# Kernel tuning notes

Hardware: AMD Instinct MI355X
Metric: run time of the kernel (lower is better)

## Reference

```python
import jax, jax.numpy as jnp
import numpy as np

B, S, H = 2, 2048, 1024
NH = 16
HD = H // NH  # 64


def _linear_params(key, fan_in, fan_out):
    k1, k2 = jax.random.split(key)
    bound = 1.0 / np.sqrt(fan_in)
    W = jax.random.uniform(k1, (fan_in, fan_out), jnp.float32, -bound, bound)
    b = jax.random.uniform(k2, (fan_out,), jnp.float32, -bound, bound)
    return W, b


def setup_inputs() -> dict:
    key = jax.random.key(0)
    ks = jax.random.split(key, 7)
    hidden_states = jax.random.normal(ks[0], (B, S, H), jnp.float32)
    governance_embeddings = jax.random.normal(ks[1], (B, H), jnp.float32)
    Wq, bq = _linear_params(ks[2], H, H)
    Wk, bk = _linear_params(ks[3], H, H)
    Wv, bv = _linear_params(ks[4], H, H)
    Wgq, bgq = _linear_params(ks[5], H, H)
    Wgk, bgk = _linear_params(ks[6], H, H)
    return {
        'hidden_states': hidden_states,
        'governance_embeddings': governance_embeddings,
        'Wq': Wq, 'bq': bq, 'Wk': Wk, 'bk': bk, 'Wv': Wv, 'bv': bv,
        'Wgq': Wgq, 'bgq': bgq, 'Wgk': Wgk, 'bgk': bgk,
    }


def reference(hidden_states, governance_embeddings, Wq, bq, Wk, bk, Wv, bv, Wgq, bgq, Wgk, bgk):
    b, s, h = hidden_states.shape
    # QKV projections -> [b, nh, s, hd]
    def heads(x):
        return x.reshape(b, s, NH, HD).transpose(0, 2, 1, 3)
    q = heads(hidden_states @ Wq + bq)
    k = heads(hidden_states @ Wk + bk)
    v = heads(hidden_states @ Wv + bv)

    scale = jnp.float32(1.0 / np.sqrt(HD))
    scores = jnp.einsum('bhid,bhjd->bhij', q, k) * scale  # [b,nh,s,s]

    # governance bias: one query per example vs per-token keys (unscaled)
    gq = (governance_embeddings @ Wgq + bgq).reshape(b, NH, HD)      # [b,nh,hd]
    gk = (hidden_states @ Wgk + bgk).reshape(b, s, NH, HD)           # [b,s,nh,hd]
    gov_scores = jnp.einsum('bhd,bshd->bhs', gq, gk)                 # [b,nh,s]

    # bias is constant along key dim (torch expand on last axis)
    combined = scores + 0.1 * gov_scores[..., :, None]

    probs = jax.nn.softmax(combined, axis=-1)  # dropout = identity (eval)
    context = jnp.einsum('bhij,bhjd->bhid', probs, v)
    context = context.transpose(0, 2, 1, 3).reshape(b, s, h)

    entropy = -jnp.sum(probs * jnp.log(probs + 1e-8), axis=-1).mean()
    influence = jnp.abs(gov_scores).mean()  # mean over expanded tensor == mean over [b,nh,s]
    concentration = probs.max(axis=-1).mean()
    return context, entropy, influence, concentration
```

## Files before the change

kernel.cpp:

```cpp
#include <hip/hip_runtime.h>


typedef unsigned short u16;
typedef __attribute__((ext_vector_type(8))) short bf16x8;
typedef __attribute__((ext_vector_type(4))) float f32x4;
typedef __attribute__((ext_vector_type(16))) float f32x16;
typedef __attribute__((ext_vector_type(2))) float f32x2;
typedef __attribute__((ext_vector_type(4))) u16 u16x4;
typedef __attribute__((ext_vector_type(4))) float float4v;
typedef __attribute__((ext_vector_type(2))) unsigned uint2v;

typedef const __attribute__((address_space(1))) void gvoid_t;
typedef __attribute__((address_space(3))) void lvoid_t;

__device__ __forceinline__ void gl_lds16(const void* g, void* l) {
  __builtin_amdgcn_global_load_lds((gvoid_t*)g, (lvoid_t*)l, 16, 0, 0);
}

__device__ __forceinline__ u16 f2bf(float x) {
  union { float f; unsigned u; } v; v.f = x;
  unsigned r = v.u + 0x7fffu + ((v.u >> 16) & 1u);
  return (u16)(r >> 16);
}
__device__ __forceinline__ float bf2f(u16 h) {
  union { unsigned u; float f; } v; v.u = ((unsigned)h) << 16; return v.f;
}
__device__ __forceinline__ unsigned pk2(float hi, float lo) {
  union { float f; unsigned u; } a, b; a.f = hi; b.f = lo;
  return __builtin_amdgcn_perm(a.u, b.u, 0x07060302u);
}
__device__ __forceinline__ bf16x8 mk8(unsigned a, unsigned b, unsigned c, unsigned d) {
  union { unsigned u[4]; bf16x8 v; } x;
  x.u[0] = a; x.u[1] = b; x.u[2] = c; x.u[3] = d; return x.v;
}

#if defined(__has_builtin)
#if __has_builtin(__builtin_amdgcn_permlane32_swap)
#define HAVE_PLSWAP 1
#endif
#if __has_builtin(__builtin_amdgcn_exp2f)
#define EXP2(x) __builtin_amdgcn_exp2f(x)
#endif
#endif
#ifndef EXP2
#define EXP2(x) exp2f(x)
#endif

__device__ __forceinline__ void plswap(unsigned& a, unsigned& b, int lane) {
#ifdef HAVE_PLSWAP
  uint2v r = __builtin_amdgcn_permlane32_swap(a, b, false, false);
  a = r.x; b = r.y;
#else
  unsigned ca = __builtin_amdgcn_ds_bpermute((lane ^ 32) << 2, a);
  unsigned cb = __builtin_amdgcn_ds_bpermute((lane ^ 32) << 2, b);
  unsigned na = (lane < 32) ? a : cb;
  unsigned nb = (lane < 32) ? ca : b;
  a = na; b = nb;
#endif
}

__global__ void prep(const float* __restrict__ hs,
                     const float* __restrict__ W0, const float* __restrict__ W1,
                     const float* __restrict__ W2, const float* __restrict__ W3,
                     const float* __restrict__ ge, const float* __restrict__ Wgq,
                     u16* __restrict__ hsB, u16* __restrict__ WB,
                     float* __restrict__ gq_part) {
  __shared__ __align__(16) u16 T[64][72];
  int bx = blockIdx.x, tid = threadIdx.x;
  if (bx < 2048) {
    int i = bx * 256 + tid;
    const float4v* in4 = (const float4v*)hs;
    float4v a = in4[i * 2], b = in4[i * 2 + 1];
    bf16x8 v;
    v[0] = (short)f2bf(a.x); v[1] = (short)f2bf(a.y);
    v[2] = (short)f2bf(a.z); v[3] = (short)f2bf(a.w);
    v[4] = (short)f2bf(b.x); v[5] = (short)f2bf(b.y);
    v[6] = (short)f2bf(b.z); v[7] = (short)f2bf(b.w);
    *(bf16x8*)&hsB[(size_t)i * 8] = v;
    return;
  }
  if (bx < 3072) {
    int idx = bx - 2048;
    int mat = idx >> 8, sub = idx & 255;
    const float* W = (mat == 0) ? W0 : (mat == 1) ? W1 : (mat == 2) ? W2 : W3;
    int k0 = (sub >> 4) * 64, n0 = (sub & 15) * 64;
#pragma unroll
    for (int p = 0; p < 4; ++p) {
      int chunk = p * 256 + tid;
      int row = chunk >> 4, cp = chunk & 15;
      float4v v = *(const float4v*)&W[(size_t)(k0 + row) * 1024 + n0 + cp * 4];
      u16x4 o; o.x = f2bf(v.x); o.y = f2bf(v.y); o.z = f2bf(v.z); o.w = f2bf(v.w);
      *(u16x4*)&T[row][cp * 4] = o;
    }
    __syncthreads();
#pragma unroll
    for (int p = 0; p < 2; ++p) {
      int chunk = p * 256 + tid;
      int nrow = chunk >> 3, cp = chunk & 7;
      bf16x8 v;
#pragma unroll
      for (int e = 0; e < 8; ++e) v[e] = (short)T[cp * 8 + e][nrow];
      *(bf16x8*)&WB[(size_t)(mat * 1024 + n0 + nrow) * 1024 + k0 + cp * 8] = v;
    }
    return;
  }
  {
    int idx = bx - 3072;
    int kb = idx >> 1, b = idx & 1;
    int col0 = tid * 4;
    float4v s = {0.f, 0.f, 0.f, 0.f};
    for (int k = kb * 32; k < kb * 32 + 32; ++k) {
      float g = ge[b * 1024 + k];
      float4v w = *(const float4v*)&Wgq[(size_t)k * 1024 + col0];
      s.x += g * w.x; s.y += g * w.y; s.z += g * w.z; s.w += g * w.w;
    }
    *(float4v*)&gq_part[(size_t)idx * 1024 + col0] = s;
  }
}

__global__ __launch_bounds__(256, 3) void gemm_qkvg(
    const u16* __restrict__ A, const u16* __restrict__ Bw,
    const float* __restrict__ bq, const float* __restrict__ bk,
    const float* __restrict__ bv, const float* __restrict__ bgk,
    const float* __restrict__ bgq, const float* __restrict__ gq_part,
    u16* __restrict__ Qb, u16* __restrict__ Kb,
    u16* __restrict__ GKb, u16* __restrict__ Vt,
    float* __restrict__ gq_final, float* __restrict__ acc3) {
  if (blockIdx.x == 1024) {
    int tid = threadIdx.x;
    if (tid < 3) acc3[tid] = 0.f;
#pragma unroll
    for (int i = 0; i < 8; ++i) {
      int t = tid + i * 256;
      float s = bgq[t & 1023];
      for (int kb = 0; kb < 32; ++kb)
        s += gq_part[(size_t)(kb * 2 + (t >> 10)) * 1024 + (t & 1023)];
      gq_final[t] = s;
    }
    return;
  }
  __shared__ __align__(16) u16 As[2][128 * 32];
  __shared__ __align__(16) u16 Bs[2][128 * 32];
  const int tid = threadIdx.x, lane = tid & 63, wv = tid >> 6;
  const int li = lane & 15, quad = lane >> 4;
  const int bid = blockIdx.x;
  const int nb = bid & 31, mb = bid >> 5;
  const u16* Ap = A + (size_t)(mb * 128) * 1024;
  const u16* Bp = Bw + (size_t)(nb * 128) * 1024;
  const int wm0 = (wv >> 1) * 64, wn0 = (wv & 1) * 64;

  f32x4 acc[4][4];
#pragma unroll
  for (int t = 0; t < 4; ++t)
#pragma unroll
    for (int u = 0; u < 4; ++u) acc[t][u] = (f32x4){0.f, 0.f, 0.f, 0.f};

#pragma unroll
  for (int jj = 0; jj < 2; ++jj) {
    int j = wv * 2 + jj;
    int row = j * 16 + (lane >> 2);
    int co = lane & 3;
    gl_lds16(Ap + (size_t)row * 1024 + co * 8, &As[0][j * 512]);
    gl_lds16(Bp + (size_t)row * 1024 + co * 8, &Bs[0][j * 512]);
  }

  for (int kt = 0; kt < 32; ++kt) {
    const int cur = kt & 1;
    __syncthreads();
    if (kt < 31) {
#pragma unroll
      for (int jj = 0; jj < 2; ++jj) {
        int j = wv * 2 + jj;
        int row = j * 16 + (lane >> 2);
        int co = lane & 3;
        gl_lds16(Ap + (size_t)row * 1024 + (kt + 1) * 32 + co * 8, &As[cur ^ 1][j * 512]);
        gl_lds16(Bp + (size_t)row * 1024 + (kt + 1) * 32 + co * 8, &Bs[cur ^ 1][j * 512]);
      }
    }
    bf16x8 af[4], bf[4];
#pragma unroll
    for (int t = 0; t < 4; ++t)
      af[t] = *(const bf16x8*)&As[cur][(wm0 + t * 16 + li) * 32 + quad * 8];
#pragma unroll
    for (int u = 0; u < 4; ++u)
      bf[u] = *(const bf16x8*)&Bs[cur][(wn0 + u * 16 + li) * 32 + quad * 8];
#pragma unroll
    for (int t = 0; t < 4; ++t)
#pragma unroll
      for (int u = 0; u < 4; ++u)
        acc[t][u] = __builtin_amdgcn_mfma_f32_16x16x32_bf16(af[t], bf[u], acc[t][u], 0, 0, 0);
  }

  const int nbase = nb * 128;
  const int mat = nbase >> 10;
  if (mat == 2) {
#pragma unroll
    for (int t = 0; t < 4; ++t)
#pragma unroll
      for (int u = 0; u < 4; ++u) {
        int col = (nbase & 1023) + wn0 + u * 16 + li;
        float bb = bv[col];
        int row = mb * 128 + wm0 + t * 16 + quad * 4;
        int b = row >> 11, s = row & 2047;
        uint2 w;
        w.x = pk2(acc[t][u][1] + bb, acc[t][u][0] + bb);
        w.y = pk2(acc[t][u][3] + bb, acc[t][u][2] + bb);
        *(uint2*)&Vt[(size_t)b * (1024 * 2048) + (size_t)col * 2048 + s] = w;
      }
  } else {
    const float* bias = (mat == 0) ? bq : (mat == 1) ? bk : bgk;
    u16* outp = (mat == 0) ? Qb : (mat == 1) ? Kb : GKb;
    const float qscale = (mat == 0) ? 0.18033688f : 1.0f;
#pragma unroll
    for (int t = 0; t < 4; ++t)
#pragma unroll
      for (int u = 0; u < 4; ++u) {
        int col = (nbase & 1023) + wn0 + u * 16 + li;
        float bb = bias[col];
#pragma unroll
        for (int r = 0; r < 4; ++r) {
          int row = mb * 128 + wm0 + t * 16 + quad * 4 + r;
          outp[(size_t)row * 1024 + col] = f2bf((acc[t][u][r] + bb) * qscale);
        }
      }
  }
}

__global__ __launch_bounds__(256, 2) void attn_kernel(
    const u16* __restrict__ Qb, const u16* __restrict__ Kb,
    const u16* __restrict__ Vt, float* __restrict__ out,
    float* __restrict__ acc3 ) {
  __shared__ __align__(16) u16 Ks[2][128 * 64];
  __shared__ __align__(16) u16 Vs[2][64 * 128];
  __shared__ float red[8];

  const int tid = threadIdx.x, lane = tid & 63, wv = tid >> 6;
  const int q_l = lane & 31, half = lane >> 5;
  const int bx = blockIdx.x;
  const int bh = bx & 31, qb = bx >> 5;
  const int b = bh >> 4, h = bh & 15;

  const u16* Qp = Qb + (size_t)(b * 2048 + qb * 128 + wv * 32 + q_l) * 1024 + h * 64;
  const u16* Kp = Kb + (size_t)(b * 2048) * 1024 + h * 64;
  const u16* Vp = Vt + (size_t)b * (1024 * 2048) + (size_t)(h * 64) * 2048;

  bf16x8 qf[4];
#pragma unroll
  for (int s = 0; s < 4; ++s)
    qf[s] = *(const bf16x8*)&Qp[s * 16 + half * 8];

  f32x2 mx2 = {-3.0e38f, -3.0e38f}, ps2 = {0.f, 0.f}, es2 = {0.f, 0.f};
  f32x16 accO[2];
#pragma unroll
  for (int dt = 0; dt < 2; ++dt)
#pragma unroll
    for (int r = 0; r < 16; ++r) accO[dt][r] = 0.f;

#pragma unroll
  for (int jj = 0; jj < 4; ++jj) {
    int j = wv * 4 + jj;
    int row = j * 8 + (lane >> 3);
    int c16 = (lane & 7) ^ (row & 7);
    gl_lds16(Kp + (size_t)row * 1024 + c16 * 8, &Ks[0][j * 512]);
  }
#pragma unroll
  for (int jj = 0; jj < 4; ++jj) {
    int j = wv * 4 + jj;
    int row = j * 4 + (lane >> 4);
    int c16 = (lane & 15) ^ (row & 7);
    gl_lds16(Vp + (size_t)row * 2048 + c16 * 8, &Vs[0][j * 512]);
  }

  for (int kt = 0; kt < 16; ++kt) {
    const int cur = kt & 1;
    __syncthreads();
    if (kt < 15) {
      const u16* Kpt = Kp + (size_t)((kt + 1) * 128) * 1024;
#pragma unroll
      for (int jj = 0; jj < 4; ++jj) {
        int j = wv * 4 + jj;
        int row = j * 8 + (lane >> 3);
        int c16 = (lane & 7) ^ (row & 7);
        gl_lds16(Kpt + (size_t)row * 1024 + c16 * 8, &Ks[cur ^ 1][j * 512]);
      }
#pragma unroll
      for (int jj = 0; jj < 4; ++jj) {
        int j = wv * 4 + jj;
        int row = j * 4 + (lane >> 4);
        int c16 = (lane & 15) ^ (row & 7);
        gl_lds16(Vp + (size_t)row * 2048 + (kt + 1) * 128 + c16 * 8, &Vs[cur ^ 1][j * 512]);
      }
    }
    const u16* KsC = &Ks[cur][0];
    const u16* VsC = &Vs[cur][0];

#pragma unroll
    for (int u = 0; u < 4; ++u) {
      f32x16 c;
#pragma unroll
      for (int r = 0; r < 16; ++r) c[r] = 0.f;
#pragma unroll
      for (int s = 0; s < 4; ++s) {
        int p = (2 * s + half) ^ (q_l & 7);
        bf16x8 a = *(const bf16x8*)&KsC[(u * 32 + q_l) * 64 + p * 8];
        c = __builtin_amdgcn_mfma_f32_32x32x16_bf16(a, qf[s], c, 0, 0, 0);
      }
#pragma unroll
      for (int r = 0; r < 8; ++r) {
        f32x2 sv = {c[2 * r], c[2 * r + 1]};
        mx2 = __builtin_elementwise_max(mx2, sv);
        f32x2 pe = {EXP2(sv.x), EXP2(sv.y)};
        ps2 += pe;
        es2 += pe * sv;
        c[2 * r] = pe.x; c[2 * r + 1] = pe.y;
      }
      unsigned p0 = pk2(c[1], c[0]),   p1 = pk2(c[3], c[2]);
      unsigned p2 = pk2(c[5], c[4]),   p3 = pk2(c[7], c[6]);
      unsigned p4 = pk2(c[9], c[8]),   p5 = pk2(c[11], c[10]);
      unsigned p6 = pk2(c[13], c[12]), p7 = pk2(c[15], c[14]);
      plswap(p0, p2, lane); plswap(p1, p3, lane);
      plswap(p4, p6, lane); plswap(p5, p7, lane);
      bf16x8 bf0 = mk8(p0, p1, p2, p3);
      bf16x8 bf1 = mk8(p4, p5, p6, p7);
#pragma unroll
      for (int dt = 0; dt < 2; ++dt) {
        int d = dt * 32 + q_l;
        int pa = (u * 4 + half) ^ (d & 7);
        int pb = (u * 4 + 2 + half) ^ (d & 7);
        bf16x8 av0 = *(const bf16x8*)&VsC[d * 128 + pa * 8];
        accO[dt] = __builtin_amdgcn_mfma_f32_32x32x16_bf16(av0, bf0, accO[dt], 0, 0, 0);
        bf16x8 av1 = *(const bf16x8*)&VsC[d * 128 + pb * 8];
        accO[dt] = __builtin_amdgcn_mfma_f32_32x32x16_bf16(av1, bf1, accO[dt], 0, 0, 0);
      }
    }
  }

  float l_st = ps2.x + ps2.y, e_st = es2.x + es2.y, m_st = fmaxf(mx2.x, mx2.y);
  float lsum = l_st + __shfl_xor(l_st, 32, 64);
  float esum = e_st + __shfl_xor(e_st, 32, 64);
  float mm = fmaxf(m_st, __shfl_xor(m_st, 32, 64));
  float inv = 1.0f / lsum;
  float entw = __logf(lsum) - 0.69314718f * esum * inv;
  float concw = EXP2(mm) * inv;

  float* outp = out + (size_t)(b * 2048 + qb * 128 + wv * 32 + q_l) * 1024 + h * 64;
#pragma unroll
  for (int dt = 0; dt < 2; ++dt)
#pragma unroll
    for (int g = 0; g < 4; ++g) {
      float4v o;
      o.x = accO[dt][4 * g + 0] * inv; o.y = accO[dt][4 * g + 1] * inv;
      o.z = accO[dt][4 * g + 2] * inv; o.w = accO[dt][4 * g + 3] * inv;
      *(float4v*)&outp[dt * 32 + 8 * g + 4 * half] = o;
    }

#pragma unroll
  for (int off = 1; off < 64; off <<= 1) {
    entw += __shfl_xor(entw, off, 64);
    concw += __shfl_xor(concw, off, 64);
  }
  if (lane == 0) { red[wv] = entw * 0.5f; red[4 + wv] = concw * 0.5f; }
  __syncthreads();
  if (tid == 0) {
    atomicAdd(&acc3[0], red[0] + red[1] + red[2] + red[3]);
    atomicAdd(&acc3[1], red[4] + red[5] + red[6] + red[7]);
  }
}

__global__ void gov_kernel(const u16* __restrict__ GKb, const float* __restrict__ gq,
                           float* __restrict__ acc_inf) {
  __shared__ float redI[4];
  int lane = threadIdx.x & 63, wv = threadIdx.x >> 6;
  int wid = blockIdx.x * 4 + wv;
  int b = wid >> 11, s = wid & 2047;
  const u16* gk = GKb + (size_t)(b * 2048 + s) * 1024 + lane * 16;
  const float* gqp = gq + b * 1024 + lane * 16;
  bf16x8 g0 = *(const bf16x8*)gk, g1 = *(const bf16x8*)(gk + 8);
  float4v q0 = *(const float4v*)&gqp[0], q1 = *(const float4v*)&gqp[4];
  float4v q2 = *(const float4v*)&gqp[8], q3 = *(const float4v*)&gqp[12];
  float sum = 0.f;
  sum += bf2f((u16)g0[0]) * q0.x + bf2f((u16)g0[1]) * q0.y +
         bf2f((u16)g0[2]) * q0.z + bf2f((u16)g0[3]) * q0.w;
  sum += bf2f((u16)g0[4]) * q1.x + bf2f((u16)g0[5]) * q1.y +
         bf2f((u16)g0[6]) * q1.z + bf2f((u16)g0[7]) * q1.w;
  sum += bf2f((u16)g1[0]) * q2.x + bf2f((u16)g1[1]) * q2.y +
         bf2f((u16)g1[2]) * q2.z + bf2f((u16)g1[3]) * q2.w;
  sum += bf2f((u16)g1[4]) * q3.x + bf2f((u16)g1[5]) * q3.y +
         bf2f((u16)g1[6]) * q3.z + bf2f((u16)g1[7]) * q3.w;
  sum += __shfl_xor(sum, 1, 64);
  sum += __shfl_xor(sum, 2, 64);
  float v = ((lane & 3) == 0) ? fabsf(sum) : 0.f;
  v += __shfl_xor(v, 4, 64);  v += __shfl_xor(v, 8, 64);
  v += __shfl_xor(v, 16, 64); v += __shfl_xor(v, 32, 64);
  if (lane == 0) redI[wv] = v;
  __syncthreads();
  if (threadIdx.x == 0)
    atomicAdd(acc_inf, redI[0] + redI[1] + redI[2] + redI[3]);
}

__global__ void finalize(const float* __restrict__ acc3, float* __restrict__ out) {
  if (threadIdx.x == 0) {
    out[0] = acc3[0] * (1.f / 65536.f);
    out[1] = acc3[2] * (1.f / 65536.f);
    out[2] = acc3[1] * (1.f / 65536.f);
  }
}

extern "C" void kernel_launch(void* const* d_in, const int* in_sizes, int n_in,
                              void* d_out, int out_size, void* d_ws, size_t ws_size,
                              hipStream_t stream) {
  (void)in_sizes; (void)n_in; (void)out_size; (void)ws_size;
  const float* hs  = (const float*)d_in[0];
  const float* ge  = (const float*)d_in[1];
  const float* Wq  = (const float*)d_in[2];
  const float* bq  = (const float*)d_in[3];
  const float* Wk  = (const float*)d_in[4];
  const float* bk  = (const float*)d_in[5];
  const float* Wv  = (const float*)d_in[6];
  const float* bv  = (const float*)d_in[7];
  const float* Wgq = (const float*)d_in[8];
  const float* bgq = (const float*)d_in[9];
  const float* Wgk = (const float*)d_in[10];
  const float* bgk = (const float*)d_in[11];

  char* ws = (char*)d_ws;
  u16* hsB = (u16*)(ws);
  u16* WB  = (u16*)(ws + (size_t)(8 << 20));
  u16* Qb  = (u16*)(ws + (size_t)(16 << 20));
  u16* Kb  = (u16*)(ws + (size_t)(24 << 20));
  u16* Vt  = (u16*)(ws + (size_t)(32 << 20));
  u16* GKb = (u16*)(ws + (size_t)(40 << 20));
  float* gq_part  = (float*)(ws + (size_t)(48 << 20));
  float* gq_final = (float*)(ws + (size_t)(48 << 20) + 262144);
  float* acc3     = (float*)(ws + (size_t)(48 << 20) + 524288);
  float* out = (float*)d_out;

  prep<<<3136, 256, 0, stream>>>(hs, Wq, Wk, Wv, Wgk, ge, Wgq, hsB, WB, gq_part);
  gemm_qkvg<<<1025, 256, 0, stream>>>(hsB, WB, bq, bk, bv, bgk, bgq, gq_part,
                                      Qb, Kb, GKb, Vt, gq_final, acc3);
  attn_kernel<<<512, 256, 0, stream>>>(Qb, Kb, Vt, out, acc3);
  gov_kernel<<<1024, 256, 0, stream>>>(GKb, gq_final, acc3 + 2);
  finalize<<<1, 64, 0, stream>>>(acc3, out + 4194304);
}
```

Measured before the change: 222.5 us.

## Fuse governance influence reduction into GEMM epilogue and drop permlane swaps in attention

The governance-key projection is no longer written to memory. Its dot product with the governance query and the absolute-value reduction now run in the GEMM epilogue, which removes the separate gov_kernel launch and the GK round trip through global memory. The gq reduction is recomputed per block in the epilogue, and the acc3 zeroing moves into prep. Separately, the attention P·V step drops the permlane32 swaps and instead gathers V fragments as 8-byte LDS reads in the matching order, trading cross-lane swaps for more, smaller LDS loads.

After: 209.5 us. 5.8% less time.

```diff
diff --git a/kernel.cpp b/kernel.cpp
--- a/kernel.cpp
+++ b/kernel.cpp
@@ -8,7 +8,6 @@
 typedef __attribute__((ext_vector_type(2))) float f32x2;
 typedef __attribute__((ext_vector_type(4))) u16 u16x4;
 typedef __attribute__((ext_vector_type(4))) float float4v;
-typedef __attribute__((ext_vector_type(2))) unsigned uint2v;
 
 typedef const __attribute__((address_space(1))) void gvoid_t;
 typedef __attribute__((address_space(3))) void lvoid_t;
@@ -35,9 +34,6 @@
 }
 
 #if defined(__has_builtin)
-#if __has_builtin(__builtin_amdgcn_permlane32_swap)
-#define HAVE_PLSWAP 1
-#endif
 #if __has_builtin(__builtin_amdgcn_exp2f)
 #define EXP2(x) __builtin_amdgcn_exp2f(x)
 #endif
@@ -46,25 +42,12 @@
 #define EXP2(x) exp2f(x)
 #endif
 
-__device__ __forceinline__ void plswap(unsigned& a, unsigned& b, int lane) {
-#ifdef HAVE_PLSWAP
-  uint2v r = __builtin_amdgcn_permlane32_swap(a, b, false, false);
-  a = r.x; b = r.y;
-#else
-  unsigned ca = __builtin_amdgcn_ds_bpermute((lane ^ 32) << 2, a);
-  unsigned cb = __builtin_amdgcn_ds_bpermute((lane ^ 32) << 2, b);
-  unsigned na = (lane < 32) ? a : cb;
-  unsigned nb = (lane < 32) ? ca : b;
-  a = na; b = nb;
-#endif
-}
-
 __global__ void prep(const float* __restrict__ hs,
                      const float* __restrict__ W0, const float* __restrict__ W1,
                      const float* __restrict__ W2, const float* __restrict__ W3,
                      const float* __restrict__ ge, const float* __restrict__ Wgq,
                      u16* __restrict__ hsB, u16* __restrict__ WB,
-                     float* __restrict__ gq_part) {
+                     float* __restrict__ gq_part, float* __restrict__ acc3) {
   __shared__ __align__(16) u16 T[64][72];
   int bx = blockIdx.x, tid = threadIdx.x;
   if (bx < 2048) {
@@ -106,6 +89,7 @@
   }
   {
     int idx = bx - 3072;
+    if (idx == 0 && tid < 3) acc3[tid] = 0.f;
     int kb = idx >> 1, b = idx & 1;
     int col0 = tid * 4;
     float4v s = {0.f, 0.f, 0.f, 0.f};
@@ -123,24 +107,11 @@
     const float* __restrict__ bq, const float* __restrict__ bk,
     const float* __restrict__ bv, const float* __restrict__ bgk,
     const float* __restrict__ bgq, const float* __restrict__ gq_part,
-    u16* __restrict__ Qb, u16* __restrict__ Kb,
-    u16* __restrict__ GKb, u16* __restrict__ Vt,
-    float* __restrict__ gq_final, float* __restrict__ acc3) {
-  if (blockIdx.x == 1024) {
-    int tid = threadIdx.x;
-    if (tid < 3) acc3[tid] = 0.f;
-#pragma unroll
-    for (int i = 0; i < 8; ++i) {
-      int t = tid + i * 256;
-      float s = bgq[t & 1023];
-      for (int kb = 0; kb < 32; ++kb)
-        s += gq_part[(size_t)(kb * 2 + (t >> 10)) * 1024 + (t & 1023)];
-      gq_final[t] = s;
-    }
-    return;
-  }
+    u16* __restrict__ Qb, u16* __restrict__ Kb, u16* __restrict__ Vt,
+    float* __restrict__ acc3) {
   __shared__ __align__(16) u16 As[2][128 * 32];
   __shared__ __align__(16) u16 Bs[2][128 * 32];
+  __shared__ float redI[4];
   const int tid = threadIdx.x, lane = tid & 63, wv = tid >> 6;
   const int li = lane & 15, quad = lane >> 4;
   const int bid = blockIdx.x;
@@ -193,7 +164,39 @@
 
   const int nbase = nb * 128;
   const int mat = nbase >> 10;
-  if (mat == 2) {
+  if (mat == 3) {
+    const int colbase = nbase & 1023;
+    const int bat = (mb * 128) >> 11;
+    float gqv[4], bgkv[4];
+#pragma unroll
+    for (int u2 = 0; u2 < 4; ++u2) {
+      int col = colbase + wn0 + u2 * 16 + li;
+      float g = bgq[col];
+      for (int kb = 0; kb < 32; ++kb)
+        g += gq_part[(size_t)(kb * 2 + bat) * 1024 + col];
+      gqv[u2] = g;
+      bgkv[u2] = bgk[col];
+    }
+    float infl = 0.f;
+#pragma unroll
+    for (int t = 0; t < 4; ++t)
+#pragma unroll
+      for (int r = 0; r < 4; ++r) {
+        float v = (acc[t][0][r] + bgkv[0]) * gqv[0];
+        v = __builtin_fmaf(acc[t][1][r] + bgkv[1], gqv[1], v);
+        v = __builtin_fmaf(acc[t][2][r] + bgkv[2], gqv[2], v);
+        v = __builtin_fmaf(acc[t][3][r] + bgkv[3], gqv[3], v);
+        v += __shfl_xor(v, 1, 64); v += __shfl_xor(v, 2, 64);
+        v += __shfl_xor(v, 4, 64); v += __shfl_xor(v, 8, 64);
+        infl += fabsf(v);
+      }
+    infl = (li == 0) ? infl : 0.f;
+    infl += __shfl_xor(infl, 16, 64);
+    infl += __shfl_xor(infl, 32, 64);
+    if (lane == 0) redI[wv] = infl;
+    __syncthreads();
+    if (tid == 0) atomicAdd(&acc3[2], redI[0] + redI[1] + redI[2] + redI[3]);
+  } else if (mat == 2) {
 #pragma unroll
     for (int t = 0; t < 4; ++t)
 #pragma unroll
@@ -208,8 +211,8 @@
         *(uint2*)&Vt[(size_t)b * (1024 * 2048) + (size_t)col * 2048 + s] = w;
       }
   } else {
-    const float* bias = (mat == 0) ? bq : (mat == 1) ? bk : bgk;
-    u16* outp = (mat == 0) ? Qb : (mat == 1) ? Kb : GKb;
+    const float* bias = (mat == 0) ? bq : bk;
+    u16* outp = (mat == 0) ? Qb : Kb;
     const float qscale = (mat == 0) ? 0.18033688f : 1.0f;
 #pragma unroll
     for (int t = 0; t < 4; ++t)
@@ -314,23 +317,22 @@
         es2 += pe * sv;
         c[2 * r] = pe.x; c[2 * r + 1] = pe.y;
       }
-      unsigned p0 = pk2(c[1], c[0]),   p1 = pk2(c[3], c[2]);
-      unsigned p2 = pk2(c[5], c[4]),   p3 = pk2(c[7], c[6]);
-      unsigned p4 = pk2(c[9], c[8]),   p5 = pk2(c[11], c[10]);
-      unsigned p6 = pk2(c[13], c[12]), p7 = pk2(c[15], c[14]);
-      plswap(p0, p2, lane); plswap(p1, p3, lane);
-      plswap(p4, p6, lane); plswap(p5, p7, lane);
-      bf16x8 bf0 = mk8(p0, p1, p2, p3);
-      bf16x8 bf1 = mk8(p4, p5, p6, p7);
+      bf16x8 bf0 = mk8(pk2(c[1], c[0]),   pk2(c[3], c[2]),
+                       pk2(c[5], c[4]),   pk2(c[7], c[6]));
+      bf16x8 bf1 = mk8(pk2(c[9], c[8]),   pk2(c[11], c[10]),
+                       pk2(c[13], c[12]), pk2(c[15], c[14]));
 #pragma unroll
       for (int dt = 0; dt < 2; ++dt) {
-        int d = dt * 32 + q_l;
-        int pa = (u * 4 + half) ^ (d & 7);
-        int pb = (u * 4 + 2 + half) ^ (d & 7);
-        bf16x8 av0 = *(const bf16x8*)&VsC[d * 128 + pa * 8];
-        accO[dt] = __builtin_amdgcn_mfma_f32_32x32x16_bf16(av0, bf0, accO[dt], 0, 0, 0);
-        bf16x8 av1 = *(const bf16x8*)&VsC[d * 128 + pb * 8];
-        accO[dt] = __builtin_amdgcn_mfma_f32_32x32x16_bf16(av1, bf1, accO[dt], 0, 0, 0);
+        int d = dt * 32 + q_l, dx = d & 7;
+        const u16* vr = &VsC[d * 128 + half * 4];
+        uint2 a0 = *(const uint2*)&vr[((u * 4 + 0) ^ dx) * 8];
+        uint2 a1 = *(const uint2*)&vr[((u * 4 + 1) ^ dx) * 8];
+        accO[dt] = __builtin_amdgcn_mfma_f32_32x32x16_bf16(
+            mk8(a0.x, a0.y, a1.x, a1.y), bf0, accO[dt], 0, 0, 0);
+        uint2 a2 = *(const uint2*)&vr[((u * 4 + 2) ^ dx) * 8];
+        uint2 a3 = *(const uint2*)&vr[((u * 4 + 3) ^ dx) * 8];
+        accO[dt] = __builtin_amdgcn_mfma_f32_32x32x16_bf16(
+            mk8(a2.x, a2.y, a3.x, a3.y), bf1, accO[dt], 0, 0, 0);
       }
     }
   }
@@ -365,37 +367,6 @@
     atomicAdd(&acc3[0], red[0] + red[1] + red[2] + red[3]);
     atomicAdd(&acc3[1], red[4] + red[5] + red[6] + red[7]);
   }
-}
-
-__global__ void gov_kernel(const u16* __restrict__ GKb, const float* __restrict__ gq,
-                           float* __restrict__ acc_inf) {
-  __shared__ float redI[4];
-  int lane = threadIdx.x & 63, wv = threadIdx.x >> 6;
-  int wid = blockIdx.x * 4 + wv;
-  int b = wid >> 11, s = wid & 2047;
-  const u16* gk = GKb + (size_t)(b * 2048 + s) * 1024 + lane * 16;
-  const float* gqp = gq + b * 1024 + lane * 16;
-  bf16x8 g0 = *(const bf16x8*)gk, g1 = *(const bf16x8*)(gk + 8);
-  float4v q0 = *(const float4v*)&gqp[0], q1 = *(const float4v*)&gqp[4];
-  float4v q2 = *(const float4v*)&gqp[8], q3 = *(const float4v*)&gqp[12];
-  float sum = 0.f;
-  sum += bf2f((u16)g0[0]) * q0.x + bf2f((u16)g0[1]) * q0.y +
-         bf2f((u16)g0[2]) * q0.z + bf2f((u16)g0[3]) * q0.w;
-  sum += bf2f((u16)g0[4]) * q1.x + bf2f((u16)g0[5]) * q1.y +
-         bf2f((u16)g0[6]) * q1.z + bf2f((u16)g0[7]) * q1.w;
-  sum += bf2f((u16)g1[0]) * q2.x + bf2f((u16)g1[1]) * q2.y +
-         bf2f((u16)g1[2]) * q2.z + bf2f((u16)g1[3]) * q2.w;
-  sum += bf2f((u16)g1[4]) * q3.x + bf2f((u16)g1[5]) * q3.y +
-         bf2f((u16)g1[6]) * q3.z + bf2f((u16)g1[7]) * q3.w;
-  sum += __shfl_xor(sum, 1, 64);
-  sum += __shfl_xor(sum, 2, 64);
-  float v = ((lane & 3) == 0) ? fabsf(sum) : 0.f;
-  v += __shfl_xor(v, 4, 64);  v += __shfl_xor(v, 8, 64);
-  v += __shfl_xor(v, 16, 64); v += __shfl_xor(v, 32, 64);
-  if (lane == 0) redI[wv] = v;
-  __syncthreads();
-  if (threadIdx.x == 0)
-    atomicAdd(acc_inf, redI[0] + redI[1] + redI[2] + redI[3]);
 }
 
 __global__ void finalize(const float* __restrict__ acc3, float* __restrict__ out) {
@@ -429,16 +400,13 @@
   u16* Qb  = (u16*)(ws + (size_t)(16 << 20));
   u16* Kb  = (u16*)(ws + (size_t)(24 << 20));
   u16* Vt  = (u16*)(ws + (size_t)(32 << 20));
-  u16* GKb = (u16*)(ws + (size_t)(40 << 20));
-  float* gq_part  = (float*)(ws + (size_t)(48 << 20));
-  float* gq_final = (float*)(ws + (size_t)(48 << 20) + 262144);
-  float* acc3     = (float*)(ws + (size_t)(48 << 20) + 524288);
+  float* gq_part = (float*)(ws + (size_t)(48 << 20));
+  float* acc3    = (float*)(ws + (size_t)(48 << 20) + 524288);
   float* out = (float*)d_out;
 
-  prep<<<3136, 256, 0, stream>>>(hs, Wq, Wk, Wv, Wgk, ge, Wgq, hsB, WB, gq_part);
-  gemm_qkvg<<<1025, 256, 0, stream>>>(hsB, WB, bq, bk, bv, bgk, bgq, gq_part,
-                                      Qb, Kb, GKb, Vt, gq_final, acc3);
+  prep<<<3136, 256, 0, stream>>>(hs, Wq, Wk, Wv, Wgk, ge, Wgq, hsB, WB, gq_part, acc3);
+  gemm_qkvg<<<1024, 256, 0, stream>>>(hsB, WB, bq, bk, bv, bgk, bgq, gq_part,
+                                      Qb, Kb, Vt, acc3);
   attn_kernel<<<512, 256, 0, stream>>>(Qb, Kb, Vt, out, acc3);
-  gov_kernel<<<1024, 256, 0, stream>>>(GKb, gq_final, acc3 + 2);
   finalize<<<1, 64, 0, stream>>>(acc3, out + 4194304);
 }
```
